# Kernel tuning notes

Hardware: AMD Instinct MI355X
Metric: run time of the kernel (lower is better)

## Reference

```python
import jax, jax.numpy as jnp
import numpy as np


def setup_inputs() -> dict:
    key = jax.random.key(0)
    ks = jax.random.split(key, 8)
    B, C, D, H, W = 4, 256, 16, 16, 16
    C8 = C // 8
    x = jax.random.normal(ks[0], (B, C, D, H, W), dtype=jnp.float32)
    # 1x1x1 conv weights == per-channel linear maps
    Wq = jax.random.normal(ks[1], (C8, C), dtype=jnp.float32) * (1.0 / np.sqrt(C))
    bq = jax.random.normal(ks[2], (C8,), dtype=jnp.float32) * 0.01
    Wk = jax.random.normal(ks[3], (C8, C), dtype=jnp.float32) * (1.0 / np.sqrt(C))
    bk = jax.random.normal(ks[4], (C8,), dtype=jnp.float32) * 0.01
    Wv = jax.random.normal(ks[5], (C, C), dtype=jnp.float32) * (1.0 / np.sqrt(C))
    bv = jax.random.normal(ks[6], (C,), dtype=jnp.float32) * 0.01
    gamma = jax.random.normal(ks[7], (1,), dtype=jnp.float32) * 0.1
    return {"x": x, "Wq": Wq, "bq": bq, "Wk": Wk, "bk": bk,
            "Wv": Wv, "bv": bv, "gamma": gamma}


def reference(x, Wq, bq, Wk, bk, Wv, bv, gamma):
    B, C, D, H, W = x.shape
    N = D * H * W
    xf = x.reshape(B, C, N)  # (B, C, N)
    # 1x1x1 convs == channel-wise linear projections
    q = jnp.einsum('qc,bcn->bnq', Wq, xf) + bq            # (B, N, C/8)
    k = jnp.einsum('kc,bcn->bkn', Wk, xf) + bk[:, None]   # (B, C/8, N)
    v = jnp.einsum('vc,bcn->bvn', Wv, xf) + bv[:, None]   # (B, C, N)
    energy = jnp.einsum('bnc,bcm->bnm', q, k)             # (B, N, N), NO 1/sqrt(d) scaling (as in source)
    attention = jax.nn.softmax(energy, axis=-1)           # softmax over keys
    # out[b,c,m] = sum_n V[b,c,n] * A[b,m,n]  (torch: bmm(V, A^T))
    out = jnp.einsum('bcn,bmn->bcm', v, attention)        # (B, C, N)
    out = out.reshape(B, C, D, H, W)
    return gamma[0] * out + x
```

## Files before the change

### kernel.cpp

```cpp
#include <hip/hip_runtime.h>
#include <hip/hip_bf16.h>
#include <math.h>

#define BATCH 4
#define CH    256
#define NPOS  4096
#define DQK   32
#define LOG2E 1.4426950408889634f
#define QB2   (-28.853900817779268f)

typedef __attribute__((ext_vector_type(8))) short bf16x8;
typedef __attribute__((ext_vector_type(4))) float f32x4;

static __device__ __forceinline__ unsigned int pack_bf2(float a, float b) {
    __hip_bfloat162 h = __float22bfloat162_rn(make_float2(a, b));
    return *reinterpret_cast<unsigned int*>(&h);
}
static __device__ __forceinline__ unsigned short f2bf1(float f) {
    unsigned int u = __float_as_uint(f);
    u += 0x7fff + ((u >> 16) & 1);
    return (unsigned short)(u >> 16);
}
static __device__ __forceinline__ bf16x8 pack8(const float* v) {
    bf16x8 r;
    #pragma unroll
    for (int j = 0; j < 8; ++j) r[j] = (short)f2bf1(v[j]);
    return r;
}

static __device__ __forceinline__ void lds_barrier() {
    asm volatile("s_waitcnt lgkmcnt(0)" ::: "memory");
    __builtin_amdgcn_s_barrier();
    asm volatile("" ::: "memory");
}
#define VWAIT0() do { asm volatile("s_waitcnt vmcnt(0)" ::: "memory"); \
                      __builtin_amdgcn_sched_barrier(0); } while (0)
#define LGKM0()  do { asm volatile("s_waitcnt lgkmcnt(0)" ::: "memory"); \
                      __builtin_amdgcn_sched_barrier(0); } while (0)

static __device__ __forceinline__ void dma16(const __hip_bfloat16* g, unsigned char* l) {
    __builtin_amdgcn_global_load_lds(
        (const __attribute__((address_space(1))) void*)g,
        (__attribute__((address_space(3))) void*)l, 16, 0, 0);
}

__global__ __launch_bounds__(256) void qkv_proj_mfma(
    const float* __restrict__ x,
    const float* __restrict__ Wq, const float* __restrict__ bq,
    const float* __restrict__ Wk, const float* __restrict__ bk,
    const float* __restrict__ Wv, const float* __restrict__ bv,
    __hip_bfloat16* __restrict__ qb, __hip_bfloat16* __restrict__ kb,
    __hip_bfloat16* __restrict__ vb)
{
    const int tid  = threadIdx.x;
    const int wave = tid >> 6, lane = tid & 63;
    const int g    = lane >> 4, lm = lane & 15;
    const int n0   = blockIdx.x * 32;
    const int b    = blockIdx.y;
    const float* xb = x + (size_t)b * CH * NPOS;

    bf16x8 xf[2][8];
    #pragma unroll
    for (int nt = 0; nt < 2; ++nt)
        #pragma unroll
        for (int kt = 0; kt < 8; ++kt) {
            const float* p = xb + (32 * kt + 8 * g) * NPOS + n0 + 16 * nt + lm;
            float v[8];
            #pragma unroll
            for (int j = 0; j < 8; ++j) v[j] = p[j * NPOS];
            xf[nt][kt] = pack8(v);
        }

    #pragma unroll
    for (int s = 0; s < 5; ++s) {
        const int cot = wave * 5 + s;
        const float* Wsrc; const float* bsrc; int cbase; int kind;
        if (cot < 2)      { Wsrc = Wq; bsrc = bq; cbase = cot * 16;      kind = 0; }
        else if (cot < 4) { Wsrc = Wk; bsrc = bk; cbase = cot * 16 - 32; kind = 1; }
        else              { Wsrc = Wv; bsrc = bv; cbase = cot * 16 - 64; kind = 2; }

        bf16x8 wf[8];
        const float* wrow = Wsrc + (size_t)(cbase + lm) * CH;
        #pragma unroll
        for (int kt = 0; kt < 8; ++kt) {
            float4 wa = *(const float4*)(wrow + 32 * kt + 8 * g);
            float4 wc = *(const float4*)(wrow + 32 * kt + 8 * g + 4);
            float wv[8] = {wa.x, wa.y, wa.z, wa.w, wc.x, wc.y, wc.z, wc.w};
            wf[kt] = pack8(wv);
        }
        const float4 b4 = *(const float4*)(bsrc + cbase + 4 * g);
        f32x4 a0 = {b4.x, b4.y, b4.z, b4.w};
        f32x4 a1 = a0;
        #pragma unroll
        for (int kt = 0; kt < 8; ++kt) {
            a0 = __builtin_amdgcn_mfma_f32_16x16x32_bf16(wf[kt], xf[0][kt], a0, 0, 0, 0);
            a1 = __builtin_amdgcn_mfma_f32_16x16x32_bf16(wf[kt], xf[1][kt], a1, 0, 0, 0);
        }
        if (kind == 0) {
            #pragma unroll
            for (int r = 0; r < 4; ++r) { a0[r] *= LOG2E; a1[r] *= LOG2E; }
        }

        if (kind <= 1) {
            __hip_bfloat16* dst = (kind == 0 ? qb : kb);
            #pragma unroll
            for (int nt = 0; nt < 2; ++nt) {
                f32x4 a = nt ? a1 : a0;
                int n = n0 + 16 * nt + lm;
                uint2 w;
                w.x = pack_bf2(a[0], a[1]);
                w.y = pack_bf2(a[2], a[3]);
                *(uint2*)(dst + ((size_t)b * NPOS + n) * DQK + cbase + 4 * g) = w;
            }
        } else {
            #pragma unroll
            for (int nt = 0; nt < 2; ++nt) {
                f32x4 a = nt ? a1 : a0;
                int n = n0 + 16 * nt + lm;
                int n64 = n >> 6, half = (n >> 5) & 1, nin = n & 31;
                #pragma unroll
                for (int r = 0; r < 4; ++r) {
                    int c = cbase + 4 * g + r;
                    size_t off = (((size_t)b * 16 + (c >> 4)) * 64 + n64) * 1024
                               + (size_t)half * 512 + (c & 15) * 32 + nin;
                    *reinterpret_cast<unsigned short*>(vb + off) = f2bf1(a[r]);
                }
            }
        }
    }
}

__global__ __launch_bounds__(512) void flash_pam_kernel(
    const __hip_bfloat16* __restrict__ qb, const __hip_bfloat16* __restrict__ kb,
    const __hip_bfloat16* __restrict__ vb, const float* __restrict__ x,
    const float* __restrict__ gamma, float* __restrict__ out)
{
    __shared__ alignas(16) unsigned char Pl[2][8192];
    __shared__ alignas(16) unsigned char Vst[8][4096];
    __shared__ alignas(16) unsigned char Kst[8][1024];
    __shared__ float lred[4][4][16];

    const int tid  = threadIdx.x;
    const int wave = tid >> 6;
    const int lane = tid & 63;
    const int g    = lane >> 4;
    const int lm   = lane & 15;
    const int bid  = blockIdx.x;
    const int b    = bid & 3;
    const int m0   = (bid >> 2) * 64;
    const int kt   = wave & 3;
    const int mtA  = (wave >> 2) * 2;
    const unsigned swz = (unsigned)(lm & 7) << 4;
    const unsigned lane16 = (unsigned)lane * 16;

    const bf16x8 qfA = *reinterpret_cast<const bf16x8*>(
        qb + ((size_t)b * NPOS + m0 + 16 * mtA + lm) * DQK + 8 * g);
    const bf16x8 qfB = *reinterpret_cast<const bf16x8*>(
        qb + ((size_t)b * NPOS + m0 + 16 * mtA + 16 + lm) * DQK + 8 * g);

    const __hip_bfloat16* kgl = kb + (size_t)b * NPOS * DQK + (16 * kt + lm) * DQK + 8 * g;
    const __hip_bfloat16* vbb = vb + (size_t)b * 16 * 64 * 1024;
    const __hip_bfloat16* vgl[4];
    #pragma unroll
    for (int cti = 0; cti < 2; ++cti)
        #pragma unroll
        for (int kc = 0; kc < 2; ++kc)
            vgl[2 * cti + kc] = vbb + (2 * wave + cti) * 65536 + kc * 512 + lm * 32 + 8 * g;
    unsigned char* vdst = &Vst[wave][0];
    unsigned char* kdst = &Kst[wave][0];

    const unsigned wbA = (unsigned)(16 * mtA + lm) * 128
                       + (((unsigned)(32 * kt + 8 * g)) ^ swz);
    const unsigned wbB = wbA + 16 * 128;
    unsigned char* P0 = &Pl[0][0];
    unsigned char* P1 = &Pl[1][0];

    f32x4 acc[2][4];
    #pragma unroll
    for (int i = 0; i < 2; ++i)
        #pragma unroll
        for (int j = 0; j < 4; ++j) acc[i][j] = (f32x4){0.f, 0.f, 0.f, 0.f};
    float lsA = 0.f, lsB = 0.f;

#define DMAK(t_) dma16(kgl + (size_t)(t_) * 2048, kdst)
#define DMAV(t_) { \
    _Pragma("unroll") for (int f = 0; f < 4; ++f) \
        dma16(vgl[f] + (size_t)(t_) * 1024, vdst + f * 1024); }
#define READK(dst) dst = *reinterpret_cast<const bf16x8*>(kdst + lane16);
#define READV(dst) { \
    _Pragma("unroll") for (int f = 0; f < 4; ++f) \
        dst[f] = *reinterpret_cast<const bf16x8*>(vdst + f * 1024 + lane16); }

#define QKW(KU, PW) { \
    f32x4 zb = {QB2, QB2, QB2, QB2}; \
    f32x4 sA = __builtin_amdgcn_mfma_f32_16x16x32_bf16(KU, qfA, zb, 0, 0, 0); \
    f32x4 sB = __builtin_amdgcn_mfma_f32_16x16x32_bf16(KU, qfB, zb, 0, 0, 0); \
    { float p0 = exp2f(sA[0]), p1 = exp2f(sA[1]); \
      float p2 = exp2f(sA[2]), p3 = exp2f(sA[3]); \
      lsA += (p0 + p1) + (p2 + p3); \
      uint2 w; w.x = pack_bf2(p0, p1); w.y = pack_bf2(p2, p3); \
      *reinterpret_cast<uint2*>((PW) + wbA) = w; } \
    { float p0 = exp2f(sB[0]), p1 = exp2f(sB[1]); \
      float p2 = exp2f(sB[2]), p3 = exp2f(sB[3]); \
      lsB += (p0 + p1) + (p2 + p3); \
      uint2 w; w.x = pack_bf2(p0, p1); w.y = pack_bf2(p2, p3); \
      *reinterpret_cast<uint2*>((PW) + wbB) = w; } }

#define PVt(PR, VR) { \
    _Pragma("unroll") for (int kc = 0; kc < 2; ++kc) { \
        bf16x8 pf[4]; \
        _Pragma("unroll") for (int mt = 0; mt < 4; ++mt) \
            pf[mt] = *reinterpret_cast<const bf16x8*>( \
                (PR) + (unsigned)(16 * mt + lm) * 128 \
                     + (((unsigned)(kc * 64 + 16 * g)) ^ swz)); \
        __builtin_amdgcn_s_setprio(1); \
        _Pragma("unroll") for (int cti = 0; cti < 2; ++cti) \
            _Pragma("unroll") for (int mt = 0; mt < 4; ++mt) \
                acc[cti][mt] = __builtin_amdgcn_mfma_f32_16x16x32_bf16( \
                    VR[2 * cti + kc], pf[mt], acc[cti][mt], 0, 0, 0); \
        __builtin_amdgcn_s_setprio(0); } }

#define BODY(t_, PR, PW) { \
    VWAIT0(); \
    bf16x8 kreg; READK(kreg); \
    bf16x8 vreg[4]; READV(vreg); \
    LGKM0(); \
    DMAV((t_) + 1); \
    { int tk2 = (t_) + 2; if (tk2 > 63) tk2 = 63; DMAK(tk2); } \
    QKW(kreg, PW); \
    PVt(PR, vreg); \
    lds_barrier(); }

    DMAK(0);
    VWAIT0();
    bf16x8 k0; READK(k0);
    LGKM0();
    DMAV(0);
    DMAK(1);
    QKW(k0, P0);
    lds_barrier();

    for (int it = 0; it < 31; ++it) {
        BODY(2 * it,     P0, P1);
        BODY(2 * it + 1, P1, P0);
    }
    BODY(62, P0, P1);

    VWAIT0();
    {
        bf16x8 vreg[4]; READV(vreg);
        PVt(P1, vreg);
    }

    lsA += __shfl_xor(lsA, 16); lsA += __shfl_xor(lsA, 32);
    lsB += __shfl_xor(lsB, 16); lsB += __shfl_xor(lsB, 32);
    if (lane < 16) {
        lred[kt][mtA][lm]     = lsA;
        lred[kt][mtA + 1][lm] = lsB;
    }
    __syncthreads();

    float linv[4];
    #pragma unroll
    for (int mt = 0; mt < 4; ++mt)
        linv[mt] = 1.f / (lred[0][mt][lm] + lred[1][mt][lm]
                        + lred[2][mt][lm] + lred[3][mt][lm]);

    const float gmv = gamma[0];
    #pragma unroll
    for (int cti = 0; cti < 2; ++cti)
        #pragma unroll
        for (int mt = 0; mt < 4; ++mt)
            #pragma unroll
            for (int r = 0; r < 4; ++r) {
                int c = 32 * wave + 16 * cti + 4 * g + r;
                size_t idx = ((size_t)b * CH + c) * NPOS + m0 + 16 * mt + lm;
                out[idx] = gmv * (acc[cti][mt][r] * linv[mt]) + x[idx];
            }
#undef BODY
#undef PVt
#undef QKW
#undef READV
#undef READK
#undef DMAV
#undef DMAK
}

extern "C" void kernel_launch(void* const* d_in, const int* in_sizes, int n_in,
                              void* d_out, int out_size, void* d_ws, size_t ws_size,
                              hipStream_t stream) {
    const float* x  = (const float*)d_in[0];
    const float* Wq = (const float*)d_in[1];
    const float* bq = (const float*)d_in[2];
    const float* Wk = (const float*)d_in[3];
    const float* bk = (const float*)d_in[4];
    const float* Wv = (const float*)d_in[5];
    const float* bv = (const float*)d_in[6];
    const float* gm = (const float*)d_in[7];
    float* out = (float*)d_out;

    __hip_bfloat16* qbuf = (__hip_bfloat16*)d_ws;
    __hip_bfloat16* kbuf = qbuf + (size_t)BATCH * NPOS * DQK;
    __hip_bfloat16* vbuf = kbuf + (size_t)BATCH * NPOS * DQK;

    qkv_proj_mfma<<<dim3(NPOS / 32, BATCH), 256, 0, stream>>>(
        x, Wq, bq, Wk, bk, Wv, bv, qbuf, kbuf, vbuf);
    flash_pam_kernel<<<dim3(NPOS / 64 * BATCH), 512, 0, stream>>>(
        qbuf, kbuf, vbuf, x, gm, out);
}
```

Baseline: 82.24 us.

## Warp-specialize attention kernel into QK/softmax producer and PV consumer waves

```diff
diff --git a/kernel.cpp b/kernel.cpp
--- a/kernel.cpp
+++ b/kernel.cpp
@@ -130,14 +130,13 @@
     }
 }
 
-__global__ __launch_bounds__(512) void flash_pam_kernel(
+__global__ __launch_bounds__(512, 2) void flash_pam_kernel(
     const __hip_bfloat16* __restrict__ qb, const __hip_bfloat16* __restrict__ kb,
     const __hip_bfloat16* __restrict__ vb, const float* __restrict__ x,
     const float* __restrict__ gamma, float* __restrict__ out)
 {
     __shared__ alignas(16) unsigned char Pl[2][8192];
-    __shared__ alignas(16) unsigned char Vst[8][4096];
-    __shared__ alignas(16) unsigned char Kst[8][1024];
+    __shared__ alignas(16) unsigned char Vst[4][8192];
     __shared__ float lred[4][4][16];
 
     const int tid  = threadIdx.x;
@@ -148,142 +147,136 @@
     const int bid  = blockIdx.x;
     const int b    = bid & 3;
     const int m0   = (bid >> 2) * 64;
-    const int kt   = wave & 3;
-    const int mtA  = (wave >> 2) * 2;
     const unsigned swz = (unsigned)(lm & 7) << 4;
     const unsigned lane16 = (unsigned)lane * 16;
-
-    const bf16x8 qfA = *reinterpret_cast<const bf16x8*>(
-        qb + ((size_t)b * NPOS + m0 + 16 * mtA + lm) * DQK + 8 * g);
-    const bf16x8 qfB = *reinterpret_cast<const bf16x8*>(
-        qb + ((size_t)b * NPOS + m0 + 16 * mtA + 16 + lm) * DQK + 8 * g);
-
-    const __hip_bfloat16* kgl = kb + (size_t)b * NPOS * DQK + (16 * kt + lm) * DQK + 8 * g;
-    const __hip_bfloat16* vbb = vb + (size_t)b * 16 * 64 * 1024;
-    const __hip_bfloat16* vgl[4];
-    #pragma unroll
-    for (int cti = 0; cti < 2; ++cti)
-        #pragma unroll
-        for (int kc = 0; kc < 2; ++kc)
-            vgl[2 * cti + kc] = vbb + (2 * wave + cti) * 65536 + kc * 512 + lm * 32 + 8 * g;
-    unsigned char* vdst = &Vst[wave][0];
-    unsigned char* kdst = &Kst[wave][0];
-
-    const unsigned wbA = (unsigned)(16 * mtA + lm) * 128
-                       + (((unsigned)(32 * kt + 8 * g)) ^ swz);
-    const unsigned wbB = wbA + 16 * 128;
     unsigned char* P0 = &Pl[0][0];
     unsigned char* P1 = &Pl[1][0];
-
-    f32x4 acc[2][4];
-    #pragma unroll
-    for (int i = 0; i < 2; ++i)
-        #pragma unroll
-        for (int j = 0; j < 4; ++j) acc[i][j] = (f32x4){0.f, 0.f, 0.f, 0.f};
-    float lsA = 0.f, lsB = 0.f;
-
-#define DMAK(t_) dma16(kgl + (size_t)(t_) * 2048, kdst)
+    const float gmv = gamma[0];
+
+    if (wave < 4) {
+        const int kt = wave;
+        bf16x8 qf[4];
+        #pragma unroll
+        for (int mt = 0; mt < 4; ++mt)
+            qf[mt] = *reinterpret_cast<const bf16x8*>(
+                qb + ((size_t)b * NPOS + m0 + 16 * mt + lm) * DQK + 8 * g);
+        const __hip_bfloat16* kgl =
+            kb + (size_t)b * NPOS * DQK + (16 * kt + lm) * DQK + 8 * g;
+        unsigned wb[4];
+        #pragma unroll
+        for (int mt = 0; mt < 4; ++mt)
+            wb[mt] = (unsigned)(16 * mt + lm) * 128
+                   + (((unsigned)(32 * kt + 8 * g)) ^ swz);
+        float ls[4] = {0.f, 0.f, 0.f, 0.f};
+
+#define QKP(KU, PW) { \
+    _Pragma("unroll") for (int mt = 0; mt < 4; ++mt) { \
+        f32x4 zb = {QB2, QB2, QB2, QB2}; \
+        f32x4 s = __builtin_amdgcn_mfma_f32_16x16x32_bf16(KU, qf[mt], zb, 0, 0, 0); \
+        float p0 = exp2f(s[0]), p1 = exp2f(s[1]); \
+        float p2 = exp2f(s[2]), p3 = exp2f(s[3]); \
+        ls[mt] += (p0 + p1) + (p2 + p3); \
+        uint2 w; w.x = pack_bf2(p0, p1); w.y = pack_bf2(p2, p3); \
+        *reinterpret_cast<uint2*>((PW) + wb[mt]) = w; } }
+
+        bf16x8 k0 = *reinterpret_cast<const bf16x8*>(kgl);
+        QKP(k0, P0);
+        bf16x8 kcur = *reinterpret_cast<const bf16x8*>(kgl + 2048);
+        lds_barrier();
+
+        for (int t = 0; t < 63; ++t) {
+            int tn = t + 2; if (tn > 63) tn = 63;
+            bf16x8 knext = *reinterpret_cast<const bf16x8*>(kgl + (size_t)tn * 2048);
+            QKP(kcur, (t & 1) ? P0 : P1);
+            kcur = knext;
+            lds_barrier();
+        }
+#undef QKP
+        #pragma unroll
+        for (int mt = 0; mt < 4; ++mt) {
+            float v = ls[mt];
+            v += __shfl_xor(v, 16);
+            v += __shfl_xor(v, 32);
+            if (lane < 16) lred[kt][mt][lm] = v;
+        }
+        lds_barrier();
+    } else {
+        const int cw = wave - 4;
+        const __hip_bfloat16* vbb = vb + (size_t)b * 16 * 64 * 1024;
+        const __hip_bfloat16* vgl[8];
+        #pragma unroll
+        for (int ct = 0; ct < 4; ++ct)
+            #pragma unroll
+            for (int kc = 0; kc < 2; ++kc)
+                vgl[2 * ct + kc] = vbb + (4 * cw + ct) * 65536 + kc * 512
+                                 + lm * 32 + 8 * g;
+        unsigned char* vdst = &Vst[cw][0];
+
+        f32x4 acc[4][4];
+        #pragma unroll
+        for (int i = 0; i < 4; ++i)
+            #pragma unroll
+            for (int j = 0; j < 4; ++j) acc[i][j] = (f32x4){0.f, 0.f, 0.f, 0.f};
+
 #define DMAV(t_) { \
-    _Pragma("unroll") for (int f = 0; f < 4; ++f) \
+    _Pragma("unroll") for (int f = 0; f < 8; ++f) \
         dma16(vgl[f] + (size_t)(t_) * 1024, vdst + f * 1024); }
-#define READK(dst) dst = *reinterpret_cast<const bf16x8*>(kdst + lane16);
-#define READV(dst) { \
-    _Pragma("unroll") for (int f = 0; f < 4; ++f) \
-        dst[f] = *reinterpret_cast<const bf16x8*>(vdst + f * 1024 + lane16); }
-
-#define QKW(KU, PW) { \
-    f32x4 zb = {QB2, QB2, QB2, QB2}; \
-    f32x4 sA = __builtin_amdgcn_mfma_f32_16x16x32_bf16(KU, qfA, zb, 0, 0, 0); \
-    f32x4 sB = __builtin_amdgcn_mfma_f32_16x16x32_bf16(KU, qfB, zb, 0, 0, 0); \
-    { float p0 = exp2f(sA[0]), p1 = exp2f(sA[1]); \
-      float p2 = exp2f(sA[2]), p3 = exp2f(sA[3]); \
-      lsA += (p0 + p1) + (p2 + p3); \
-      uint2 w; w.x = pack_bf2(p0, p1); w.y = pack_bf2(p2, p3); \
-      *reinterpret_cast<uint2*>((PW) + wbA) = w; } \
-    { float p0 = exp2f(sB[0]), p1 = exp2f(sB[1]); \
-      float p2 = exp2f(sB[2]), p3 = exp2f(sB[3]); \
-      lsB += (p0 + p1) + (p2 + p3); \
-      uint2 w; w.x = pack_bf2(p0, p1); w.y = pack_bf2(p2, p3); \
-      *reinterpret_cast<uint2*>((PW) + wbB) = w; } }
-
-#define PVt(PR, VR) { \
-    _Pragma("unroll") for (int kc = 0; kc < 2; ++kc) { \
-        bf16x8 pf[4]; \
+
+#define PVPHASE(PR) { \
+    bf16x8 vreg[8]; \
+    _Pragma("unroll") for (int f = 0; f < 8; ++f) \
+        vreg[f] = *reinterpret_cast<const bf16x8*>(vdst + f * 1024 + lane16); \
+    bf16x8 pf[2][4]; \
+    _Pragma("unroll") for (int kc = 0; kc < 2; ++kc) \
         _Pragma("unroll") for (int mt = 0; mt < 4; ++mt) \
-            pf[mt] = *reinterpret_cast<const bf16x8*>( \
+            pf[kc][mt] = *reinterpret_cast<const bf16x8*>( \
                 (PR) + (unsigned)(16 * mt + lm) * 128 \
                      + (((unsigned)(kc * 64 + 16 * g)) ^ swz)); \
-        __builtin_amdgcn_s_setprio(1); \
-        _Pragma("unroll") for (int cti = 0; cti < 2; ++cti) \
-            _Pragma("unroll") for (int mt = 0; mt < 4; ++mt) \
-                acc[cti][mt] = __builtin_amdgcn_mfma_f32_16x16x32_bf16( \
-                    VR[2 * cti + kc], pf[mt], acc[cti][mt], 0, 0, 0); \
-        __builtin_amdgcn_s_setprio(0); } }
-
-#define BODY(t_, PR, PW) { \
-    VWAIT0(); \
-    bf16x8 kreg; READK(kreg); \
-    bf16x8 vreg[4]; READV(vreg); \
     LGKM0(); \
-    DMAV((t_) + 1); \
-    { int tk2 = (t_) + 2; if (tk2 > 63) tk2 = 63; DMAK(tk2); } \
-    QKW(kreg, PW); \
-    PVt(PR, vreg); \
-    lds_barrier(); }
-
-    DMAK(0);
-    VWAIT0();
-    bf16x8 k0; READK(k0);
-    LGKM0();
-    DMAV(0);
-    DMAK(1);
-    QKW(k0, P0);
-    lds_barrier();
-
-    for (int it = 0; it < 31; ++it) {
-        BODY(2 * it,     P0, P1);
-        BODY(2 * it + 1, P1, P0);
+    DMA_NEXT; \
+    __builtin_amdgcn_s_setprio(1); \
+    _Pragma("unroll") for (int ct = 0; ct < 4; ++ct) \
+        _Pragma("unroll") for (int mt = 0; mt < 4; ++mt) \
+            _Pragma("unroll") for (int kc = 0; kc < 2; ++kc) \
+                acc[ct][mt] = __builtin_amdgcn_mfma_f32_16x16x32_bf16( \
+                    vreg[2 * ct + kc], pf[kc][mt], acc[ct][mt], 0, 0, 0); \
+    __builtin_amdgcn_s_setprio(0); }
+
+        DMAV(0);
+        lds_barrier();
+
+        for (int t = 0; t < 63; ++t) {
+            VWAIT0();
+#define DMA_NEXT DMAV(t + 1)
+            PVPHASE((t & 1) ? P1 : P0);
+#undef DMA_NEXT
+            lds_barrier();
+        }
+        VWAIT0();
+#define DMA_NEXT
+        PVPHASE(P1);
+#undef DMA_NEXT
+        lds_barrier();
+
+        float linv[4];
+        #pragma unroll
+        for (int mt = 0; mt < 4; ++mt)
+            linv[mt] = 1.f / (lred[0][mt][lm] + lred[1][mt][lm]
+                            + lred[2][mt][lm] + lred[3][mt][lm]);
+
+        #pragma unroll
+        for (int ct = 0; ct < 4; ++ct)
+            #pragma unroll
+            for (int mt = 0; mt < 4; ++mt)
+                #pragma unroll
+                for (int r = 0; r < 4; ++r) {
+                    int c = 64 * cw + 16 * ct + 4 * g + r;
+                    size_t idx = ((size_t)b * CH + c) * NPOS + m0 + 16 * mt + lm;
+                    out[idx] = gmv * (acc[ct][mt][r] * linv[mt]) + x[idx];
+                }
+#undef PVPHASE
+#undef DMAV
     }
-    BODY(62, P0, P1);
-
-    VWAIT0();
-    {
-        bf16x8 vreg[4]; READV(vreg);
-        PVt(P1, vreg);
-    }
-
-    lsA += __shfl_xor(lsA, 16); lsA += __shfl_xor(lsA, 32);
-    lsB += __shfl_xor(lsB, 16); lsB += __shfl_xor(lsB, 32);
-    if (lane < 16) {
-        lred[kt][mtA][lm]     = lsA;
-        lred[kt][mtA + 1][lm] = lsB;
-    }
-    __syncthreads();
-
-    float linv[4];
-    #pragma unroll
-    for (int mt = 0; mt < 4; ++mt)
-        linv[mt] = 1.f / (lred[0][mt][lm] + lred[1][mt][lm]
-                        + lred[2][mt][lm] + lred[3][mt][lm]);
-
-    const float gmv = gamma[0];
-    #pragma unroll
-    for (int cti = 0; cti < 2; ++cti)
-        #pragma unroll
-        for (int mt = 0; mt < 4; ++mt)
-            #pragma unroll
-            for (int r = 0; r < 4; ++r) {
-                int c = 32 * wave + 16 * cti + 4 * g + r;
-                size_t idx = ((size_t)b * CH + c) * NPOS + m0 + 16 * mt + lm;
-                out[idx] = gmv * (acc[cti][mt][r] * linv[mt]) + x[idx];
-            }
-#undef BODY
-#undef PVt
-#undef QKW
-#undef READV
-#undef READK
-#undef DMAV
-#undef DMAK
 }
 
 extern "C" void kernel_launch(void* const* d_in, const int* in_sizes, int n_in,
```

After: 80.58 us. -2.0%, faster.
